# Performance work log

Hardware: AMD Instinct MI355X
Metric: run time of the kernel (lower is better)

The kernel has to match this reference:

```python
import jax, jax.numpy as jnp
import numpy as np

REGION_NUM = 16
B, C, H, W = 16, 3, 512, 512


def setup_inputs() -> dict:
    key = jax.random.key(0)
    k1, k2 = jax.random.split(key)
    x = jax.random.normal(k1, (B, C, H, W), dtype=jnp.float32)
    # torch.rand(total_splits) hoisted out of forward for determinism:
    # shape (b*c, region_num - 1)
    rand_perc = jax.random.uniform(k2, (B * C, REGION_NUM - 1), dtype=jnp.float32)
    return {"x": x, "rand_perc": rand_perc}


def reference(x, rand_perc):
    b, c, h, w = x.shape
    bc = b * c
    x_flat = x.reshape(bc, h, w)                       # (bc, h, w)

    flat = x_flat.reshape(bc, -1)
    min_val = flat.min(axis=1)                         # (bc,)
    max_val = flat.max(axis=1)                         # (bc,)

    # region boundaries: unsorted random splits, as in the original
    splits = rand_perc * (max_val - min_val)[:, None] + min_val[:, None]  # (bc, R-1)
    left = jnp.concatenate([min_val[:, None], splits], axis=1)            # (bc, R)
    right = jnpp if False else jnp.concatenate([splits, (max_val + 1e-6)[:, None]], axis=1)  # (bc, R)

    # per-pixel region mask, argmax picks first matching region
    x_exp = x_flat[:, None, :, :]                      # (bc, 1, h, w)
    mask = (x_exp >= left[:, :, None, None]) & (x_exp < right[:, :, None, None])  # (bc, R, h, w)
    idx = jnp.argmax(mask, axis=1)                     # (bc, h, w)

    # gather lower boundary per pixel
    quant = jnp.take_along_axis(left, idx.reshape(bc, -1), axis=1).reshape(bc, h, w)
    return quant.reshape(b, c, h, w)
```

## Files before the change

kernel.cpp:

```cpp
#include <hip/hip_runtime.h>
#include <math.h>

#define IMGS 48
#define IMG_ELEMS (512*512)
#define BLOCKS_A_PER_IMG 64
#define BLOCKS_C_PER_IMG 64

__global__ __launch_bounds__(256) void minmax_kernel(const float* __restrict__ x,
                                                     float* __restrict__ pmin,
                                                     float* __restrict__ pmax) {
    int blk = blockIdx.x;
    int img = blk >> 6;
    int b   = blk & 63;
    const float4* xin = (const float4*)x + (size_t)img * (IMG_ELEMS / 4) + (size_t)b * 1024;
    int t = threadIdx.x;

    float mn = INFINITY, mx = -INFINITY;
#pragma unroll
    for (int k = 0; k < 4; ++k) {
        float4 d = xin[k * 256 + t];
        mn = fminf(mn, fminf(fminf(d.x, d.y), fminf(d.z, d.w)));
        mx = fmaxf(mx, fmaxf(fmaxf(d.x, d.y), fmaxf(d.z, d.w)));
    }
#pragma unroll
    for (int off = 32; off >= 1; off >>= 1) {
        mn = fminf(mn, __shfl_xor(mn, off));
        mx = fmaxf(mx, __shfl_xor(mx, off));
    }
    __shared__ float smn[4], smx[4];
    int wave = t >> 6;
    if ((t & 63) == 0) { smn[wave] = mn; smx[wave] = mx; }
    __syncthreads();
    if (t == 0) {
        pmin[blk] = fminf(fminf(smn[0], smn[1]), fminf(smn[2], smn[3]));
        pmax[blk] = fmaxf(fmaxf(smx[0], smx[1]), fmaxf(smx[2], smx[3]));
    }
}

__global__ __launch_bounds__(256) void quant_fused(const float* __restrict__ x,
                                                   const float* __restrict__ pmin,
                                                   const float* __restrict__ pmax,
                                                   const float* __restrict__ rp,
                                                   float* __restrict__ out) {
    int blk  = blockIdx.x;
    int img  = blk >> 6;
    int b    = blk & 63;
    int t    = threadIdx.x;
    int lane = t & 63;
    int wave = t >> 6;

    __shared__ float sorted[17];
    __shared__ float s_sb[15], s_vv[16];

    size_t base = (size_t)img * (IMG_ELEMS / 4) + (size_t)b * 1024 + t;
    const float4* xin = (const float4*)x + base;
    float4 d0 = xin[0];
    float4 d1 = xin[256];
    float4 d2 = xin[512];
    float4 d3 = xin[768];

    if (wave == 0) {
        float mn = pmin[img * 64 + lane];
        float mx = pmax[img * 64 + lane];
#pragma unroll
        for (int off = 32; off >= 1; off >>= 1) {
            mn = fminf(mn, __shfl_xor(mn, off));
            mx = fmaxf(mx, __shfl_xor(mx, off));
        }
        float maxeps = __fadd_rn(mx, 1e-6f);

        float u = (lane >= 1 && lane <= 15) ? rp[img * 15 + (lane - 1)] : 0.0f;
        float split = __fadd_rn(__fmul_rn(u, __fsub_rn(mx, mn)), mn);
        float bval  = (lane == 0) ? mn : (lane == 16 ? maxeps : split);

        int rank = 0;
#pragma unroll
        for (int i = 0; i < 17; ++i) {
            float vi = __shfl(bval, i);
            rank += (vi < bval) || (vi == bval && i < lane);
        }
        if (lane < 17) sorted[rank] = bval;

        float tg = sorted[lane & 15];
        float v  = __shfl(bval, 0);
        bool found = false;
#pragma unroll
        for (int r = 0; r < 16; ++r) {
            float Lr = __shfl(bval, r);
            float Rr = __shfl(bval, r + 1);
            bool c = (tg >= Lr) && (tg < Rr);
            v = (c && !found) ? Lr : v;
            found = found || c;
        }
        if (lane < 16)  s_vv[lane] = v;
        if (lane < 15)  s_sb[lane] = sorted[lane + 1];
    }
    __syncthreads();

    float sb[15], vv[16];
#pragma unroll
    for (int k = 0; k < 15; ++k) sb[k] = s_sb[k];
#pragma unroll
    for (int k = 0; k < 16; ++k) vv[k] = s_vv[k];

    float4* oput = (float4*)out + base;
    float4 din[4] = {d0, d1, d2, d3};
#pragma unroll
    for (int k = 0; k < 4; ++k) {
        float4 d = din[k];
        float ox = vv[0], oy = vv[0], oz = vv[0], ow = vv[0];
#pragma unroll
        for (int j = 1; j < 16; ++j) {
            ox = (d.x >= sb[j - 1]) ? vv[j] : ox;
            oy = (d.y >= sb[j - 1]) ? vv[j] : oy;
            oz = (d.z >= sb[j - 1]) ? vv[j] : oz;
            ow = (d.w >= sb[j - 1]) ? vv[j] : ow;
        }
        oput[k * 256] = make_float4(ox, oy, oz, ow);
    }
}

extern "C" void kernel_launch(void* const* d_in, const int* in_sizes, int n_in,
                              void* d_out, int out_size, void* d_ws, size_t ws_size,
                              hipStream_t stream) {
    const float* x  = (const float*)d_in[0];
    const float* rp = (const float*)d_in[1];
    float* out = (float*)d_out;
    float* ws  = (float*)d_ws;

    float* pmin = ws;
    float* pmax = ws + 3072;

    minmax_kernel<<<IMGS * BLOCKS_A_PER_IMG, 256, 0, stream>>>(x, pmin, pmax);
    quant_fused<<<IMGS * BLOCKS_C_PER_IMG, 256, 0, stream>>>(x, pmin, pmax, rp, out);
}
```

Measured before the change: 110.9 us.

## Fuse min/max and quantization into one cooperative kernel with grid sync

Replaces the two-kernel pipeline with a single cooperative kernel. Each block loads its 16 float4s per thread into registers, reduces min/max, publishes partials, does a grid-wide sync, then quantizes from the held registers, so x is read from memory once instead of twice. The cost is a grid barrier and high register pressure (64 floats of data per thread) with the grid sized so all blocks stay resident at once. If the cooperative launch fails it falls back to the old two kernels.

```diff
diff --git a/kernel.cpp b/kernel.cpp
--- a/kernel.cpp
+++ b/kernel.cpp
@@ -1,10 +1,115 @@
 #include <hip/hip_runtime.h>
+#include <hip/hip_cooperative_groups.h>
 #include <math.h>
 
+namespace cg = cooperative_groups;
+
 #define IMGS 48
-#define IMG_ELEMS (512*512)
-#define BLOCKS_A_PER_IMG 64
-#define BLOCKS_C_PER_IMG 64
+#define BLOCKS_PER_IMG 16
+#define GRID_BLOCKS (IMGS * BLOCKS_PER_IMG)
+#define F4_PER_THREAD 16
+
+__global__ __launch_bounds__(256, 3) void lbq_onepass(const float* __restrict__ x,
+                                                      const float* __restrict__ rp,
+                                                      float* __restrict__ out,
+                                                      float* pmin,
+                                                      float* pmax) {
+    int blk  = blockIdx.x;
+    int img  = blk >> 4;
+    int b    = blk & 15;
+    int t    = threadIdx.x;
+    int lane = t & 63;
+    int wave = t >> 6;
+
+    size_t base = (size_t)img * 65536 + (size_t)b * 4096 + t;
+    const float4* xin = (const float4*)x + base;
+    float4 d[F4_PER_THREAD];
+#pragma unroll
+    for (int k = 0; k < F4_PER_THREAD; ++k) d[k] = xin[k * 256];
+
+    float mn = INFINITY, mx = -INFINITY;
+#pragma unroll
+    for (int k = 0; k < F4_PER_THREAD; ++k) {
+        mn = fminf(mn, fminf(fminf(d[k].x, d[k].y), fminf(d[k].z, d[k].w)));
+        mx = fmaxf(mx, fmaxf(fmaxf(d[k].x, d[k].y), fmaxf(d[k].z, d[k].w)));
+    }
+#pragma unroll
+    for (int off = 32; off >= 1; off >>= 1) {
+        mn = fminf(mn, __shfl_xor(mn, off));
+        mx = fmaxf(mx, __shfl_xor(mx, off));
+    }
+    __shared__ float smn[4], smx[4];
+    if (lane == 0) { smn[wave] = mn; smx[wave] = mx; }
+    __syncthreads();
+    if (t == 0) {
+        atomicExch(&pmin[blk], fminf(fminf(smn[0], smn[1]), fminf(smn[2], smn[3])));
+        atomicExch(&pmax[blk], fmaxf(fmaxf(smx[0], smx[1]), fmaxf(smx[2], smx[3])));
+    }
+
+    cg::this_grid().sync();
+
+    __shared__ float sorted[17];
+    __shared__ float s_sb[15], s_vv[16];
+    if (wave == 0) {
+        float pmn = atomicAdd(&pmin[img * 16 + (lane & 15)], 0.0f);
+        float pmx = atomicAdd(&pmax[img * 16 + (lane & 15)], 0.0f);
+#pragma unroll
+        for (int off = 8; off >= 1; off >>= 1) {
+            pmn = fminf(pmn, __shfl_xor(pmn, off));
+            pmx = fmaxf(pmx, __shfl_xor(pmx, off));
+        }
+        float m0 = pmn, M0 = pmx;
+        float maxeps = __fadd_rn(M0, 1e-6f);
+
+        float u = (lane >= 1 && lane <= 15) ? rp[img * 15 + (lane - 1)] : 0.0f;
+        float split = __fadd_rn(__fmul_rn(u, __fsub_rn(M0, m0)), m0);
+        float bval  = (lane == 0) ? m0 : (lane == 16 ? maxeps : split);
+
+        int rank = 0;
+#pragma unroll
+        for (int i = 0; i < 17; ++i) {
+            float vi = __shfl(bval, i);
+            rank += (vi < bval) || (vi == bval && i < lane);
+        }
+        if (lane < 17) sorted[rank] = bval;
+
+        float tg = sorted[lane & 15];
+        float v  = __shfl(bval, 0);
+        bool found = false;
+#pragma unroll
+        for (int r = 0; r < 16; ++r) {
+            float Lr = __shfl(bval, r);
+            float Rr = __shfl(bval, r + 1);
+            bool c = (tg >= Lr) && (tg < Rr);
+            v = (c && !found) ? Lr : v;
+            found = found || c;
+        }
+        if (lane < 16)  s_vv[lane] = v;
+        if (lane < 15)  s_sb[lane] = sorted[lane + 1];
+    }
+    __syncthreads();
+
+    float sb[15], vv[16];
+#pragma unroll
+    for (int k = 0; k < 15; ++k) sb[k] = s_sb[k];
+#pragma unroll
+    for (int k = 0; k < 16; ++k) vv[k] = s_vv[k];
+
+    float4* oput = (float4*)out + base;
+#pragma unroll
+    for (int k = 0; k < F4_PER_THREAD; ++k) {
+        float4 e = d[k];
+        float ox = vv[0], oy = vv[0], oz = vv[0], ow = vv[0];
+#pragma unroll
+        for (int j = 1; j < 16; ++j) {
+            ox = (e.x >= sb[j - 1]) ? vv[j] : ox;
+            oy = (e.y >= sb[j - 1]) ? vv[j] : oy;
+            oz = (e.z >= sb[j - 1]) ? vv[j] : oz;
+            ow = (e.w >= sb[j - 1]) ? vv[j] : ow;
+        }
+        oput[k * 256] = make_float4(ox, oy, oz, ow);
+    }
+}
 
 __global__ __launch_bounds__(256) void minmax_kernel(const float* __restrict__ x,
                                                      float* __restrict__ pmin,
@@ -12,7 +117,7 @@
     int blk = blockIdx.x;
     int img = blk >> 6;
     int b   = blk & 63;
-    const float4* xin = (const float4*)x + (size_t)img * (IMG_ELEMS / 4) + (size_t)b * 1024;
+    const float4* xin = (const float4*)x + (size_t)img * 65536 + (size_t)b * 1024;
     int t = threadIdx.x;
 
     float mn = INFINITY, mx = -INFINITY;
@@ -52,7 +157,7 @@
     __shared__ float sorted[17];
     __shared__ float s_sb[15], s_vv[16];
 
-    size_t base = (size_t)img * (IMG_ELEMS / 4) + (size_t)b * 1024 + t;
+    size_t base = (size_t)img * 65536 + (size_t)b * 1024 + t;
     const float4* xin = (const float4*)x + base;
     float4 d0 = xin[0];
     float4 d1 = xin[256];
@@ -68,7 +173,6 @@
             mx = fmaxf(mx, __shfl_xor(mx, off));
         }
         float maxeps = __fadd_rn(mx, 1e-6f);
-
         float u = (lane >= 1 && lane <= 15) ? rp[img * 15 + (lane - 1)] : 0.0f;
         float split = __fadd_rn(__fmul_rn(u, __fsub_rn(mx, mn)), mn);
         float bval  = (lane == 0) ? mn : (lane == 16 ? maxeps : split);
@@ -125,12 +229,17 @@
                               hipStream_t stream) {
     const float* x  = (const float*)d_in[0];
     const float* rp = (const float*)d_in[1];
-    float* out = (float*)d_out;
-    float* ws  = (float*)d_ws;
-
+    float* out  = (float*)d_out;
+    float* ws   = (float*)d_ws;
     float* pmin = ws;
-    float* pmax = ws + 3072;
-
-    minmax_kernel<<<IMGS * BLOCKS_A_PER_IMG, 256, 0, stream>>>(x, pmin, pmax);
-    quant_fused<<<IMGS * BLOCKS_C_PER_IMG, 256, 0, stream>>>(x, pmin, pmax, rp, out);
-}
+    float* pmax = ws + 4096;
+
+    void* args[] = {(void*)&x, (void*)&rp, (void*)&out, (void*)&pmin, (void*)&pmax};
+    hipError_t err = hipLaunchCooperativeKernel((const void*)lbq_onepass,
+                                                dim3(GRID_BLOCKS), dim3(256),
+                                                args, 0, stream);
+    if (err != hipSuccess) {
+        minmax_kernel<<<IMGS * 64, 256, 0, stream>>>(x, pmin, pmax);
+        quant_fused<<<IMGS * 64, 256, 0, stream>>>(x, pmin, pmax, rp, out);
+    }
+}
```

After: 215.6 us. +94.4%, slower.
